# Performance work log

Measured on AMD Instinct MI355X. Metric: run time of the kernel, lower is better.

Reference implementation:

```python
import jax, jax.numpy as jnp
import numpy as np

B, T, N, CIN, C, L, NC, S = 8, 64, 200, 200, 128, 2, 2, 100
SPARSITY = 30


def bn(x, g, b, eps=1e-5):
    # BatchNorm1d forward with batch statistics (training-mode math, biased var)
    m = x.mean(0)
    v = x.var(0)
    return (x - m) / jnp.sqrt(v + eps) * g + b


def ln(x, g, b, eps=1e-5):
    m = x.mean(-1, keepdims=True)
    v = x.var(-1, keepdims=True)
    return (x - m) / jnp.sqrt(v + eps) * g + b


def setup_inputs() -> dict:
    key = jax.random.key(0)
    ks = iter(jax.random.split(key, 64))

    def nrm(shape, s=0.02):
        return jax.random.normal(next(ks), shape, jnp.float32) * s

    return dict(
        fMRI_v=jax.random.normal(next(ks), (B, T, N, CIN), jnp.float32),
        fMRI_a=jax.random.uniform(next(ks), (B, T, N, N), jnp.float32),
        sMRI_trad=jax.random.normal(next(ks), (B, S), jnp.float32),
        sMRI_deep=jnp.zeros((B, 1, 8, 8, 8), jnp.float32),
        csatt=1, CA_MOD=0,
        w_init=nrm((CIN, C)), b_init=jnp.zeros((C,), jnp.float32),
        gin_eps=jnp.zeros((L,), jnp.float32),
        gin_w1=nrm((L, C, C)), gin_b1=jnp.zeros((L, C), jnp.float32),
        gin_bn1_g=jnp.ones((L, C), jnp.float32), gin_bn1_b=jnp.zeros((L, C), jnp.float32),
        gin_w2=nrm((L, C, C)), gin_b2=jnp.zeros((L, C), jnp.float32),
        gin_bn2_g=jnp.ones((L, C), jnp.float32), gin_bn2_b=jnp.zeros((L, C), jnp.float32),
        sero_w=nrm((L, C, C)), sero_b=jnp.zeros((L, C), jnp.float32),
        sero_bn_g=jnp.ones((L, C), jnp.float32), sero_bn_b=jnp.zeros((L, C), jnp.float32),
        sero_aw=nrm((L, C, N)), sero_ab=jnp.zeros((L, N), jnp.float32),
        tr_wqkv=nrm((L, C, 3 * C)), tr_bqkv=jnp.zeros((L, 3 * C), jnp.float32),
        tr_wo=nrm((L, C, C)), tr_bo=jnp.zeros((L, C), jnp.float32),
        tr_ln1_g=jnp.ones((L, C), jnp.float32), tr_ln1_b=jnp.zeros((L, C), jnp.float32),
        tr_ln2_g=jnp.ones((L, C), jnp.float32), tr_ln2_b=jnp.zeros((L, C), jnp.float32),
        tr_w1=nrm((L, C, 2 * C)), tr_b1=jnp.zeros((L, 2 * C), jnp.float32),
        tr_w2=nrm((L, 2 * C, C)), tr_b2=jnp.zeros((L, C), jnp.float32),
        cls_w=nrm((L, C, NC)), cls_b=jnp.zeros((L, NC), jnp.float32),
        smri_w=nrm((S, C)), smri_b=jnp.zeros((C,), jnp.float32),
        smri_bn_g=jnp.ones((C,), jnp.float32), smri_bn_b=jnp.zeros((C,), jnp.float32),
    )


def reference(fMRI_v, fMRI_a, sMRI_trad, sMRI_deep, csatt, CA_MOD,
              w_init, b_init, gin_eps,
              gin_w1, gin_b1, gin_bn1_g, gin_bn1_b,
              gin_w2, gin_b2, gin_bn2_g, gin_bn2_b,
              sero_w, sero_b, sero_bn_g, sero_bn_b, sero_aw, sero_ab,
              tr_wqkv, tr_bqkv, tr_wo, tr_bo,
              tr_ln1_g, tr_ln1_b, tr_ln2_g, tr_ln2_b,
              tr_w1, tr_b1, tr_w2, tr_b2,
              cls_w, cls_b, smri_w, smri_b, smri_bn_g, smri_bn_b):
    b, t, n = fMRI_a.shape[:3]
    # initial linear over flattened (b t n) tokens
    h3 = (fMRI_v.reshape(-1, fMRI_v.shape[-1]) @ w_init + b_init).reshape(b, t, n, -1)
    # _collate_adjacency: per-(sample,timepoint) percentile threshold -> block-diag sparse
    # with all-ones values; equivalent to a batched masked matmul.
    thr = jnp.percentile(fMRI_a, 100 - SPARSITY, axis=(-2, -1), keepdims=True)
    mask = (fMRI_a > thr).astype(h3.dtype)  # [b,t,n,n]

    logit = jnp.zeros((b, cls_w.shape[-1]), h3.dtype)
    latents, node_attns, time_attns = [], [], []
    scale = 1.0 / jnp.sqrt(jnp.asarray(h3.shape[-1], h3.dtype))
    for l in range(L):
        # LayerGIN: note the original feeds h3 (initial features) to EVERY layer
        agg = jnp.einsum('btij,btjc->btic', mask, h3) + gin_eps[l] * h3
        x = agg.reshape(-1, agg.shape[-1])
        x = jax.nn.relu(bn(x @ gin_w1[l] + gin_b1[l], gin_bn1_g[l], gin_bn1_b[l]))
        x = jax.nn.relu(bn(x @ gin_w2[l] + gin_b2[l], gin_bn2_g[l], gin_bn2_b[l]))
        hb = x.reshape(b, t, n, -1).transpose(1, 0, 2, 3)  # (t,b,n,c)
        # ModuleSERO readout (node_axis=2)
        xr = hb.mean(2)  # (t,b,c)
        e = jax.nn.gelu(bn(xr.reshape(t * b, -1) @ sero_w[l] + sero_b[l],
                           sero_bn_g[l], sero_bn_b[l]), approximate=False)
        ga = jax.nn.sigmoid(e @ sero_aw[l] + sero_ab[l]).reshape(t, b, n)
        hr = (hb * ga[..., None]).mean(2)  # (t,b,c)
        node_attns.append(ga.transpose(1, 0, 2))  # (b,t,n)
        # ModuleTransformer (single head, post-LN, no residual before ln1)
        qkv = hr @ tr_wqkv[l] + tr_bqkv[l]
        q, k, v = jnp.split(qkv, 3, axis=-1)
        A = jax.nn.softmax(jnp.einsum('tbc,sbc->bts', q, k) * scale, axis=-1)  # (b,t,t)
        att = jnp.einsum('bts,sbc->tbc', A, v) @ tr_wo[l] + tr_bo[l]
        x1 = ln(att, tr_ln1_g[l], tr_ln1_b[l])
        m = jax.nn.relu(x1 @ tr_w1[l] + tr_b1[l]) @ tr_w2[l] + tr_b2[l]
        x2 = ln(x1 + m, tr_ln2_g[l], tr_ln2_b[l])
        time_attns.append(A)
        lat = x2.sum(0)  # cls_token='sum' over time
        logit = logit + lat @ cls_w[l] + cls_b[l]
        latents.append(lat)
    feat_fMRI = jnp.stack(latents, 1).mean(1)  # (b,c)
    feat_sMRI = bn(sMRI_trad @ smri_w + smri_b, smri_bn_g, smri_bn_b)
    node_attn = jnp.stack(node_attns, 1)  # (b,L,t,n)
    time_attn = jnp.stack(time_attns, 1)  # (b,L,t,t)
    return (logit, feat_fMRI, feat_sMRI, node_attn, time_attn)
```

## Files before the change

kernel.cpp:

```cpp
#include <hip/hip_runtime.h>
#include <math.h>

#define B_   8
#define T_   64
#define N_   200
#define CIN_ 200
#define C_   128
#define L_   2
#define NC_  2
#define S_   100
#define BT_  512
#define RB_  102400

typedef __attribute__((ext_vector_type(8))) short short8v;
typedef __attribute__((ext_vector_type(4))) float f32x4v;

union U4S8 { uint4 u; short8v s; };

__device__ __forceinline__ unsigned short f2bf(float f) {
    unsigned u = __float_as_uint(f);
    unsigned r = (u + 0x7FFFu + ((u >> 16) & 1u)) >> 16;
    return (unsigned short)r;
}
__device__ __forceinline__ float bf2f(unsigned short u) {
    return __uint_as_float(((unsigned)u) << 16);
}
__device__ __forceinline__ float bflo(unsigned u) { return __uint_as_float(u << 16); }
__device__ __forceinline__ float bfhi(unsigned u) { return __uint_as_float(u & 0xFFFF0000u); }
__device__ __forceinline__ unsigned packbf(float a, float b) {
    return (unsigned)f2bf(a) | ((unsigned)f2bf(b) << 16);
}

#define GLL(src, dst) __builtin_amdgcn_global_load_lds( \
    (const __attribute__((address_space(1))) unsigned int*)(src), \
    (__attribute__((address_space(3))) unsigned int*)(dst), 16, 0, 0)

__global__ __launch_bounds__(1024) void thr_kernel(const float* __restrict__ a,
                                                   float* __restrict__ thr,
                                                   unsigned* __restrict__ msk) {
    __shared__ int      hist[1024];
    __shared__ int      red[1024];
    __shared__ unsigned smask[1400];
    __shared__ float    candV[6144];
    __shared__ unsigned short candP[6144];
    __shared__ int      part[256];
    __shared__ int      grp[32];
    __shared__ float    cand2[256];
    __shared__ int      meta[8];
    __shared__ float    s_thr;
    int tid = threadIdx.x, lane = tid & 63;
    int bt = blockIdx.x;
    hist[tid] = 0;
    for (int i = tid; i < 1400; i += 1024) smask[i] = 0u;
    if (tid == 0) { meta[0] = 0; meta[1] = 0; }
    __syncthreads();

    const float4* x4 = (const float4*)(a + (long)bt * 40000);
    int c_lo = 0;
    #pragma unroll 1
    for (int it = 0; it < 10; it++) {
        int i4 = tid + it * 1024;
        unsigned nhi = 0u, ncm = 0u;
        float vv[4] = {0.f, 0.f, 0.f, 0.f};
        if (i4 < 10000) {
            float4 v = x4[i4];
            vv[0] = v.x; vv[1] = v.y; vv[2] = v.z; vv[3] = v.w;
            #pragma unroll
            for (int j = 0; j < 4; j++) {
                float f = vv[j];
                if (f < 0.65f) c_lo++;
                else if (f < 0.75f) ncm |= 1u << j;
                else nhi |= 1u << j;
            }
            if (nhi) {
                int vi = i4 * 4;
                int row = vi / 200, col = vi - row * 200;
                atomicOr(&smask[row * 7 + (col >> 5)], nhi << (col & 31));
            }
        }
        int cnt = __popc(ncm);
        int pfx = cnt;
        #pragma unroll
        for (int d = 1; d < 64; d <<= 1) {
            int t = __shfl_up(pfx, d, 64);
            if (lane >= d) pfx += t;
        }
        int total = __shfl(pfx, 63, 64);
        if (total) {
            int bw = 0;
            if (lane == 63) bw = atomicAdd(&meta[0], total);
            bw = __shfl(bw, 63, 64);
            int p = bw + pfx - cnt;
            #pragma unroll
            for (int j = 0; j < 4; j++) {
                if ((ncm >> j) & 1u) {
                    float f = vv[j];
                    if (p < 6144) { candV[p] = f; candP[p] = (unsigned short)(i4 * 4 + j); }
                    int bin = (int)((f - 0.65f) * 10240.0f);
                    bin = bin < 0 ? 0 : (bin > 1023 ? 1023 : bin);
                    atomicAdd(&hist[bin], 1);
                    p++;
                }
            }
        }
    }
    red[tid] = c_lo;
    __syncthreads();
    for (int off = 512; off; off >>= 1) {
        if (tid < off) red[tid] += red[tid + off];
        __syncthreads();
    }
    int c_lo_tot = red[0];
    if (tid < 256) part[tid] = hist[4*tid] + hist[4*tid+1] + hist[4*tid+2] + hist[4*tid+3];
    __syncthreads();
    if (tid < 32) {
        int s = 0;
        for (int i = 0; i < 8; i++) s += part[8*tid + i];
        grp[tid] = s;
    }
    __syncthreads();
    if (tid == 0) {
        int r = 27999 - c_lo_tot;
        int cum = 0, g = 0;
        while (cum + grp[g] <= r) cum += grp[g++];
        int t = g * 8;
        while (cum + part[t] <= r) cum += part[t++];
        int b = t * 4;
        while (cum + hist[b] <= r) cum += hist[b++];
        meta[2] = b; meta[3] = cum;
        int r1 = r + 1;
        cum = 0; g = 0;
        while (cum + grp[g] <= r1) cum += grp[g++];
        t = g * 8;
        while (cum + part[t] <= r1) cum += part[t++];
        b = t * 4;
        while (cum + hist[b] <= r1) cum += hist[b++];
        meta[4] = b; meta[5] = r;
    }
    __syncthreads();
    int blo = meta[2], base = meta[3], bhi = meta[4], r = meta[5];
    int m = meta[0]; if (m > 6144) m = 6144;
    for (int i = tid; i < m; i += 1024) {
        float v = candV[i];
        int bin = (int)((v - 0.65f) * 10240.0f);
        bin = bin < 0 ? 0 : (bin > 1023 ? 1023 : bin);
        if (bin >= blo && bin <= bhi) {
            int p = atomicAdd(&meta[1], 1);
            if (p < 256) cand2[p] = v;
        }
    }
    __syncthreads();
    if (tid == 0) {
        int m2 = meta[1]; if (m2 > 256) m2 = 256;
        for (int i = 1; i < m2; i++) {
            float key = cand2[i]; int j = i - 1;
            while (j >= 0 && cand2[j] > key) { cand2[j+1] = cand2[j]; j--; }
            cand2[j+1] = key;
        }
        float s1 = cand2[r - base], s2 = cand2[r + 1 - base];
        float tv = s1 * 0.701171875f + s2 * 0.298828125f;
        thr[bt] = tv;
        s_thr = tv;
    }
    __syncthreads();
    float tv = s_thr;
    for (int i = tid; i < m; i += 1024) {
        if (candV[i] > tv) {
            int vi = candP[i];
            int row = vi / 200, col = vi - row * 200;
            atomicOr(&smask[row * 7 + (col >> 5)], 1u << (col & 31));
        }
    }
    __syncthreads();
    for (int i = tid; i < 1400; i += 1024)
        msk[(long)bt * 1400 + i] = smask[i];
}

__global__ void wtcvt5_kernel(const float* __restrict__ w_init,
                              const float* __restrict__ gin_w1,
                              const float* __restrict__ gin_w2,
                              unsigned short* __restrict__ WT0,
                              unsigned short* __restrict__ WT1,
                              unsigned short* __restrict__ WT2) {
    int grp = blockIdx.x >> 7, c = blockIdx.x & 127;
    const float* w; unsigned short* wt; int K, Kpad;
    if (grp == 0)      { w = w_init;                     wt = WT0;                     K = 200; Kpad = 224; }
    else if (grp <= 2) { w = gin_w1 + (grp - 1) * C_ * C_; wt = WT1 + (grp - 1) * 128 * 128; K = 128; Kpad = 128; }
    else               { w = gin_w2 + (grp - 3) * C_ * C_; wt = WT2 + (grp - 3) * 128 * 128; K = 128; Kpad = 128; }
    for (int k = threadIdx.x; k < Kpad; k += 64)
        wt[(long)c * Kpad + k] = f2bf((k < K) ? w[(long)k * 128 + c] : 0.f);
}

__global__ __launch_bounds__(256) void bngemm_kernel(
        const unsigned short* __restrict__ xb,
        const unsigned short* __restrict__ wt,
        const float* __restrict__ bias, const float* __restrict__ statsIn,
        const float* __restrict__ bng, const float* __restrict__ bnb,
        unsigned short* __restrict__ y, float* __restrict__ statsOut) {
    __shared__ unsigned char pool[65536];
    __shared__ float bnS[128], bnB[128];
    int tid = threadIdx.x;
    int wave = tid >> 6, lane = tid & 63, quad = lane >> 4, m16 = lane & 15;
    long row0g = (long)blockIdx.x * 128;

    {
        int r0 = tid >> 2;
        int csw = (tid & 3) ^ ((r0 >> 1) & 3);
        int r1 = 64 + (tid >> 2);
        int csw1 = (tid & 3) ^ ((r1 >> 1) & 3);
        #pragma unroll
        for (int ks = 0; ks < 4; ks++) {
            char* Adst = (char*)pool + ks * 16384;
            char* Bdst = Adst + 8192;
            GLL((const char*)xb + ((row0g + r0) * 128 + ks * 32) * 2 + csw * 16,
                Adst + wave * 1024);
            GLL((const char*)xb + ((row0g + r1) * 128 + ks * 32) * 2 + csw1 * 16,
                Adst + 4096 + wave * 1024);
            GLL((const char*)wt + (long)r0 * 256 + ks * 64 + csw * 16,
                Bdst + wave * 1024);
            GLL((const char*)wt + (long)r1 * 256 + ks * 64 + csw1 * 16,
                Bdst + 4096 + wave * 1024);
        }
    }
    if (tid < 128) {
        float mm = statsIn[tid] * (1.f / (float)RB_);
        float var = fmaxf(statsIn[128 + tid] * (1.f / (float)RB_) - mm * mm, 0.f);
        float sc = bng[tid] / sqrtf(var + 1e-5f);
        bnS[tid] = sc; bnB[tid] = bnb[tid] - mm * sc;
    }
    f32x4v acc[2][8];
    #pragma unroll
    for (int i = 0; i < 2; i++)
        #pragma unroll
        for (int j = 0; j < 8; j++) acc[i][j] = (f32x4v){0.f, 0.f, 0.f, 0.f};

    __syncthreads();

    #pragma unroll 1
    for (int ks = 0; ks < 4; ks++) {
        const char* Ab = (const char*)pool + ks * 16384;
        const char* Bb = Ab + 8192;
        int kf = ks * 32 + quad * 8;
        U4S8 bU[8];
        #pragma unroll
        for (int nt = 0; nt < 8; nt++) {
            int r = nt * 16 + m16;
            int ch = quad ^ ((r >> 1) & 3);
            bU[nt].u = *(const uint4*)(Bb + r * 64 + ch * 16);
        }
        U4S8 aU[2];
        #pragma unroll
        for (int mt = 0; mt < 2; mt++) {
            int r = wave * 32 + mt * 16 + m16;
            int ch = quad ^ ((r >> 1) & 3);
            aU[mt].u = *(const uint4*)(Ab + r * 64 + ch * 16);
        }
        float4 s0 = *(const float4*)&bnS[kf], s1 = *(const float4*)&bnS[kf + 4];
        float4 b0 = *(const float4*)&bnB[kf], b1 = *(const float4*)&bnB[kf + 4];
        #pragma unroll
        for (int mt = 0; mt < 2; mt++) {
            uint4 u = aU[mt].u;
            float f0 = fmaxf(bflo(u.x) * s0.x + b0.x, 0.f);
            float f1 = fmaxf(bfhi(u.x) * s0.y + b0.y, 0.f);
            float f2 = fmaxf(bflo(u.y) * s0.z + b0.z, 0.f);
            float f3 = fmaxf(bfhi(u.y) * s0.w + b0.w, 0.f);
            float f4 = fmaxf(bflo(u.z) * s1.x + b1.x, 0.f);
            float f5 = fmaxf(bfhi(u.z) * s1.y + b1.y, 0.f);
            float f6 = fmaxf(bflo(u.w) * s1.z + b1.z, 0.f);
            float f7 = fmaxf(bfhi(u.w) * s1.w + b1.w, 0.f);
            u.x = packbf(f0, f1); u.y = packbf(f2, f3);
            u.z = packbf(f4, f5); u.w = packbf(f6, f7);
            aU[mt].u = u;
        }
        #pragma unroll
        for (int nt = 0; nt < 8; nt++) {
            acc[0][nt] = __builtin_amdgcn_mfma_f32_16x16x32_bf16(aU[0].s, bU[nt].s, acc[0][nt], 0, 0, 0);
            acc[1][nt] = __builtin_amdgcn_mfma_f32_16x16x32_bf16(aU[1].s, bU[nt].s, acc[1][nt], 0, 0, 0);
        }
    }

    __syncthreads();
    unsigned short* trans = (unsigned short*)pool;
    float sAcc[8], qAcc[8];
    #pragma unroll
    for (int nt = 0; nt < 8; nt++) {
        int col = nt * 16 + m16;
        float bv = bias[col];
        float s = 0.f, q = 0.f;
        #pragma unroll
        for (int mt = 0; mt < 2; mt++) {
            int lrb = wave * 32 + mt * 16 + quad * 4;
            #pragma unroll
            for (int i = 0; i < 4; i++) {
                int lr = lrb + i;
                float v = acc[mt][nt][i] + bv;
                trans[lr * 128 + (col ^ ((lr & 6) << 2))] = f2bf(v);
                s += v; q += v * v;
            }
        }
        sAcc[nt] = s; qAcc[nt] = q;
    }
    __syncthreads();
    #pragma unroll
    for (int rnd = 0; rnd < 8; rnd++) {
        int row = rnd * 16 + (tid >> 4), ch = tid & 15;
        uint4 v = *(const uint4*)&trans[row * 128 + ((ch * 8) ^ ((row & 6) << 2))];
        *(uint4*)&y[(row0g + row) * 128 + ch * 8] = v;
    }
    __syncthreads();
    float* redS = (float*)pool;
    float* redQ = redS + 2048;
    #pragma unroll
    for (int nt = 0; nt < 8; nt++) {
        int col = nt * 16 + m16;
        redS[col * 16 + wave * 4 + quad] = sAcc[nt];
        redQ[col * 16 + wave * 4 + quad] = qAcc[nt];
    }
    __syncthreads();
    if (tid < 128) {
        float s = 0.f, q = 0.f;
        #pragma unroll
        for (int j = 0; j < 16; j++) { s += redS[tid * 16 + j]; q += redQ[tid * 16 + j]; }
        atomicAdd(&statsOut[tid], s);
        atomicAdd(&statsOut[128 + tid], q);
    }
}

__global__ __launch_bounds__(256) void h3gemmT_kernel(
        const float* __restrict__ xv, const unsigned short* __restrict__ wt,
        const float* __restrict__ bias,
        unsigned short* __restrict__ yrow, unsigned short* __restrict__ zt) {
    __shared__ unsigned char pool[49152];
    int tid = threadIdx.x;
    int wave = tid >> 6, lane = tid & 63, quad = lane >> 4, m16 = lane & 15;
    long row0g = (long)blockIdx.x * 128;

    auto STAGE = [&](int buf, int ks) {
        #pragma unroll
        for (int j = 0; j < 2; j++) {
            int r = j * 64 + (tid >> 2);
            int c = (tid & 3) ^ ((r >> 1) & 3);
            const char* src = (const char*)wt + (long)r * 448 + ks * 64 + c * 16;
            char* dst = (char*)pool + 32768 + buf * 8192 + j * 4096 + wave * 1024;
            GLL(src, dst);
        }
        const char* xb = (const char*)xv;
        #pragma unroll
        for (int j = 0; j < 4; j++) {
            int r = j * 32 + (tid >> 3);
            int c = (tid & 7) ^ (r & 7);
            const char* src = xb + ((row0g + r) * 200 + ks * 32) * 4 + c * 16;
            char* dst = (char*)pool + buf * 16384 + j * 4096 + wave * 1024;
            GLL(src, dst);
        }
    };

    f32x4v acc[2][8];
    #pragma unroll
    for (int i = 0; i < 2; i++)
        #pragma unroll
        for (int j = 0; j < 8; j++) acc[i][j] = (f32x4v){0.f, 0.f, 0.f, 0.f};

    STAGE(0, 0);
    __syncthreads();

    for (int ks = 0; ks < 6; ks++) {
        if (ks + 1 < 6) {
            STAGE((ks + 1) & 1, ks + 1);
            asm volatile("s_waitcnt vmcnt(6)" ::: "memory");
        } else {
            asm volatile("s_waitcnt vmcnt(0)" ::: "memory");
        }
        __builtin_amdgcn_s_barrier();
        asm volatile("" ::: "memory");

        const char* Ab = (const char*)pool + (ks & 1) * 16384;
        const char* Bb = (const char*)pool + 32768 + (ks & 1) * 8192;
        U4S8 bU[8];
        #pragma unroll
        for (int nt = 0; nt < 8; nt++) {
            int r = nt * 16 + m16;
            int ch = quad ^ ((r >> 1) & 3);
            bU[nt].u = *(const uint4*)(Bb + r * 64 + ch * 16);
        }
        U4S8 aU[2];
        #pragma unroll
        for (int mt = 0; mt < 2; mt++) {
            int r = wave * 32 + mt * 16 + m16;
            int swz = r & 7;
            const char* base = Ab + r * 128;
            float4 v0 = *(const float4*)(base + ((2 * quad) ^ swz) * 16);
            float4 v1 = *(const float4*)(base + ((2 * quad + 1) ^ swz) * 16);
            uint4 o;
            o.x = packbf(v0.x, v0.y); o.y = packbf(v0.z, v0.w);
            o.z = packbf(v1.x, v1.y); o.w = packbf(v1.z, v1.w);
            aU[mt].u = o;
        }
        #pragma unroll
        for (int nt = 0; nt < 8; nt++) {
            acc[0][nt] = __builtin_amdgcn_mfma_f32_16x16x32_bf16(aU[0].s, bU[nt].s, acc[0][nt], 0, 0, 0);
            acc[1][nt] = __builtin_amdgcn_mfma_f32_16x16x32_bf16(aU[1].s, bU[nt].s, acc[1][nt], 0, 0, 0);
        }
        asm volatile("s_waitcnt lgkmcnt(0)" ::: "memory");
        __builtin_amdgcn_s_barrier();
        asm volatile("" ::: "memory");
    }
    {
        int kf = 192 + quad * 8;
        U4S8 bU[8];
        #pragma unroll
        for (int nt = 0; nt < 8; nt++)
            bU[nt].u = *(const uint4*)&wt[(long)(nt * 16 + m16) * 224 + kf];
        U4S8 aU[2];
        #pragma unroll
        for (int mt = 0; mt < 2; mt++) {
            uint4 o = {0u, 0u, 0u, 0u};
            if (kf + 8 <= 200) {
                const float* p = &xv[(row0g + wave * 32 + mt * 16 + m16) * 200 + kf];
                float4 v0 = *(const float4*)p;
                float4 v1 = *(const float4*)(p + 4);
                o.x = packbf(v0.x, v0.y); o.y = packbf(v0.z, v0.w);
                o.z = packbf(v1.x, v1.y); o.w = packbf(v1.z, v1.w);
            }
            aU[mt].u = o;
        }
        #pragma unroll
        for (int nt = 0; nt < 8; nt++) {
            acc[0][nt] = __builtin_amdgcn_mfma_f32_16x16x32_bf16(aU[0].s, bU[nt].s, acc[0][nt], 0, 0, 0);
            acc[1][nt] = __builtin_amdgcn_mfma_f32_16x16x32_bf16(aU[1].s, bU[nt].s, acc[1][nt], 0, 0, 0);
        }
    }

    unsigned short* tile = (unsigned short*)pool;
    #pragma unroll
    for (int nt = 0; nt < 8; nt++) {
        int col = nt * 16 + m16;
        float bv = bias[col];
        #pragma unroll
        for (int mt = 0; mt < 2; mt++) {
            int lrb = wave * 32 + mt * 16 + quad * 4;
            #pragma unroll
            for (int i = 0; i < 4; i++) {
                int lr = lrb + i;
                tile[lr * 128 + (col ^ ((lr & 14) << 2))] = f2bf(acc[mt][nt][i] + bv);
            }
        }
    }
    __syncthreads();
    #pragma unroll
    for (int rnd = 0; rnd < 8; rnd++) {
        int row = rnd * 16 + (tid >> 4), ch = tid & 15;
        uint4 v = *(const uint4*)&tile[row * 128 + ((ch * 8) ^ ((row & 14) << 2))];
        *(uint4*)&yrow[(row0g + row) * 128 + ch * 8] = v;
    }
    int r0 = blockIdx.x * 128;
    int bt0 = r0 / 200, n0 = r0 - bt0 * 200;
    int len0 = 200 - n0; if (len0 > 128) len0 = 128;
    int c = tid & 127, h = tid >> 7;
    #pragma unroll
    for (int u = 0; u < 8; u++) {
        int rl = h * 64 + u * 8;
        unsigned short e[8];
        #pragma unroll
        for (int j = 0; j < 8; j++)
            e[j] = tile[(rl + j) * 128 + (c ^ (((rl + j) & 14) << 2))];
        uint4 o;
        o.x = (unsigned)e[0] | ((unsigned)e[1] << 16);
        o.y = (unsigned)e[2] | ((unsigned)e[3] << 16);
        o.z = (unsigned)e[4] | ((unsigned)e[5] << 16);
        o.w = (unsigned)e[6] | ((unsigned)e[7] << 16);
        int bt, n;
        if (rl < len0) { bt = bt0; n = n0 + rl; } else { bt = bt0 + 1; n = rl - len0; }
        *(uint4*)&zt[((long)bt * 128 + c) * 224 + n] = o;
    }
    if (n0 >= 72) {
        uint4 z = {0u, 0u, 0u, 0u};
        for (int idx = tid; idx < 384; idx += 256) {
            int c2 = idx & 127, u2 = idx >> 7;
            *(uint4*)&zt[((long)bt0 * 128 + c2) * 224 + 200 + u2 * 8] = z;
        }
    }
}

__global__ __launch_bounds__(256) void maskfused_kernel(
        const unsigned* __restrict__ msk, const unsigned short* __restrict__ zt,
        const unsigned short* __restrict__ h3, const unsigned short* __restrict__ w1t,
        const float* __restrict__ geps, int l, const float* __restrict__ b1,
        unsigned short* __restrict__ y, float* __restrict__ statsOut) {
    __shared__ unsigned char pool[65536];
    __shared__ unsigned sbits[128 * 7];
    int tid = threadIdx.x;
    int bt = blockIdx.x & 511, half = blockIdx.x >> 9;
    int row0 = half * 128;
    int wave = tid >> 6, lane = tid & 63, quad = lane >> 4, m16 = lane & 15;
    const char* ztb = (const char*)(zt + (long)bt * 128 * 224);

    {
        int r0 = tid >> 2;
        int q0 = (tid & 3) ^ ((r0 >> 1) & 3);
        int r1 = 64 + (tid >> 2);
        int q1 = (tid & 3) ^ ((r1 >> 1) & 3);
        #pragma unroll
        for (int kc = 0; kc < 7; kc++) {
            char* dst = (char*)pool + kc * 8192;
            GLL(ztb + r0 * 448 + kc * 64 + q0 * 16, dst + wave * 1024);
            GLL(ztb + r1 * 448 + kc * 64 + q1 * 16, dst + 4096 + wave * 1024);
        }
    }
    for (int idx = tid; idx < 896; idx += 256) {
        int gr = row0 + idx / 7;
        sbits[idx] = (gr < N_) ? msk[(long)bt * 1400 + gr * 7 + (idx % 7)] : 0u;
    }
    unsigned ONEu = 0x3F80u;

    f32x4v acc[2][8];
    #pragma unroll
    for (int i = 0; i < 2; i++)
        #pragma unroll
        for (int j = 0; j < 8; j++) acc[i][j] = (f32x4v){0.f, 0.f, 0.f, 0.f};

    __syncthreads();

    #pragma unroll 1
    for (int kc = 0; kc < 7; kc++) {
        const char* sb = (const char*)pool + kc * 8192;
        U4S8 bU[8];
        #pragma unroll
        for (int nt = 0; nt < 8; nt++) {
            int r = nt * 16 + m16;
            int q = quad ^ ((r >> 1) & 3);
            bU[nt].u = *(const uint4*)(sb + r * 64 + q * 16);
        }
        U4S8 aU[2];
        #pragma unroll
        for (int mt = 0; mt < 2; mt++) {
            int lr = wave * 32 + mt * 16 + m16;
            unsigned bits = (sbits[lr * 7 + kc] >> (quad * 8)) & 0xFFu;
            unsigned o[4];
            #pragma unroll
            for (int p = 0; p < 4; p++) {
                unsigned lo = ((bits >> (2 * p)) & 1u) ? ONEu : 0u;
                unsigned hi = ((bits >> (2 * p + 1)) & 1u) ? ONEu : 0u;
                o[p] = lo | (hi << 16);
            }
            aU[mt].u = make_uint4(o[0], o[1], o[2], o[3]);
        }
        #pragma unroll
        for (int nt = 0; nt < 8; nt++) {
            acc[0][nt] = __builtin_amdgcn_mfma_f32_16x16x32_bf16(aU[0].s, bU[nt].s, acc[0][nt], 0, 0, 0);
            acc[1][nt] = __builtin_amdgcn_mfma_f32_16x16x32_bf16(aU[1].s, bU[nt].s, acc[1][nt], 0, 0, 0);
        }
    }
    __syncthreads();

    unsigned short* magg = (unsigned short*)pool;
    unsigned short* trans = (unsigned short*)(pool + 32768);
    #pragma unroll
    for (int nt = 0; nt < 8; nt++) {
        int col = nt * 16 + m16;
        #pragma unroll
        for (int mt = 0; mt < 2; mt++) {
            int lrb = wave * 32 + mt * 16 + quad * 4;
            #pragma unroll
            for (int i = 0; i < 4; i++) {
                int lr = lrb + i;
                magg[lr * 128 + (col ^ ((lr & 6) << 2))] = f2bf(acc[mt][nt][i]);
            }
        }
    }
    __syncthreads();

    float eps = geps[l];
    f32x4v acc2[2][8];
    #pragma unroll
    for (int i = 0; i < 2; i++)
        #pragma unroll
        for (int j = 0; j < 8; j++) acc2[i][j] = (f32x4v){0.f, 0.f, 0.f, 0.f};

    #pragma unroll 1
    for (int ks = 0; ks < 4; ks++) {
        int kf = ks * 32 + quad * 8;
        U4S8 bU[8];
        #pragma unroll
        for (int nt = 0; nt < 8; nt++)
            bU[nt].u = *(const uint4*)&w1t[(long)(nt * 16 + m16) * 128 + kf];
        U4S8 aU[2];
        #pragma unroll
        for (int mt = 0; mt < 2; mt++) {
            int r = wave * 32 + mt * 16 + m16;
            uint4 mu = *(const uint4*)&magg[r * 128 + (kf ^ ((r & 6) << 2))];
            int gr = row0 + r;
            uint4 hu = {0u, 0u, 0u, 0u};
            if (gr < N_) hu = *(const uint4*)&h3[((long)bt * N_ + gr) * 128 + kf];
            float f0 = bflo(mu.x) + eps * bflo(hu.x);
            float f1 = bfhi(mu.x) + eps * bfhi(hu.x);
            float f2 = bflo(mu.y) + eps * bflo(hu.y);
            float f3 = bfhi(mu.y) + eps * bfhi(hu.y);
            float f4 = bflo(mu.z) + eps * bflo(hu.z);
            float f5 = bfhi(mu.z) + eps * bfhi(hu.z);
            float f6 = bflo(mu.w) + eps * bflo(hu.w);
            float f7 = bfhi(mu.w) + eps * bfhi(hu.w);
            uint4 o;
            o.x = packbf(f0, f1); o.y = packbf(f2, f3);
            o.z = packbf(f4, f5); o.w = packbf(f6, f7);
            aU[mt].u = o;
        }
        #pragma unroll
        for (int nt = 0; nt < 8; nt++) {
            acc2[0][nt] = __builtin_amdgcn_mfma_f32_16x16x32_bf16(aU[0].s, bU[nt].s, acc2[0][nt], 0, 0, 0);
            acc2[1][nt] = __builtin_amdgcn_mfma_f32_16x16x32_bf16(aU[1].s, bU[nt].s, acc2[1][nt], 0, 0, 0);
        }
    }

    float sAcc[8], qAcc[8];
    #pragma unroll
    for (int nt = 0; nt < 8; nt++) {
        int col = nt * 16 + m16;
        float bv = b1[col];
        float s = 0.f, q = 0.f;
        #pragma unroll
        for (int mt = 0; mt < 2; mt++) {
            int lrb = wave * 32 + mt * 16 + quad * 4;
            #pragma unroll
            for (int i = 0; i < 4; i++) {
                int lr = lrb + i;
                float v = acc2[mt][nt][i] + bv;
                trans[lr * 128 + (col ^ ((lr & 6) << 2))] = f2bf(v);
                if (row0 + lr < N_) { s += v; q += v * v; }
            }
        }
        sAcc[nt] = s; qAcc[nt] = q;
    }
    __syncthreads();
    #pragma unroll
    for (int rnd = 0; rnd < 8; rnd++) {
        int row = rnd * 16 + (tid >> 4), ch = tid & 15;
        int gr = row0 + row;
        uint4 v = *(const uint4*)&trans[row * 128 + ((ch * 8) ^ ((row & 6) << 2))];
        if (gr < N_)
            *(uint4*)&y[((long)bt * N_ + gr) * 128 + ch * 8] = v;
    }
    __syncthreads();
    float* redS = (float*)(pool + 32768);
    float* redQ = redS + 2048;
    #pragma unroll
    for (int nt = 0; nt < 8; nt++) {
        int col = nt * 16 + m16;
        redS[col * 16 + wave * 4 + quad] = sAcc[nt];
        redQ[col * 16 + wave * 4 + quad] = qAcc[nt];
    }
    __syncthreads();
    if (tid < 128) {
        float s = 0.f, q = 0.f;
        #pragma unroll
        for (int j = 0; j < 16; j++) { s += redS[tid * 16 + j]; q += redQ[tid * 16 + j]; }
        atomicAdd(&statsOut[tid], s);
        atomicAdd(&statsOut[128 + tid], q);
    }
}

__global__ __launch_bounds__(256) void xrE_kernel(
        const unsigned short* __restrict__ raw, const float* __restrict__ stats,
        const float* __restrict__ g, const float* __restrict__ b,
        const float* __restrict__ sw, const float* __restrict__ sb,
        float* __restrict__ E, float* __restrict__ statE) {
    __shared__ float red[256];
    __shared__ float xrrow[128];
    int tid = threadIdx.x, c = tid & 127, hf = tid >> 7;
    int t = blockIdx.x / B_, bb = blockIdx.x % B_;
    const unsigned short* base = raw + ((long)bb * T_ + t) * N_ * C_;
    float m = stats[c] * (1.f / (float)RB_);
    float var = fmaxf(stats[128 + c] * (1.f / (float)RB_) - m * m, 0.f);
    float sc = g[c] / sqrtf(var + 1e-5f);
    float sh = b[c] - m * sc;
    float s = 0.f;
    for (int n = hf * 100; n < hf * 100 + 100; n++)
        s += fmaxf(fmaf(bf2f(base[n * C_ + c]), sc, sh), 0.f);
    red[tid] = s;
    __syncthreads();
    if (hf == 0) xrrow[c] = (red[c] + red[c + 128]) * (1.f / 200.f);
    __syncthreads();
    float acc = 0.f;
    for (int k = hf * 64; k < hf * 64 + 64; k++)
        acc = fmaf(xrrow[k], sw[k * C_ + c], acc);
    red[tid] = acc;
    __syncthreads();
    if (hf == 0) {
        float v = red[c] + red[c + 128] + sb[c];
        E[(long)blockIdx.x * C_ + c] = v;
        atomicAdd(&statE[c], v);
        atomicAdd(&statE[C_ + c], v * v);
    }
}

__global__ __launch_bounds__(256) void ga_kernel(const float* __restrict__ eRaw,
                          const float* __restrict__ stats,
                          const float* __restrict__ sg, const float* __restrict__ sb,
                          const float* __restrict__ aw, const float* __restrict__ ab,
                          float* __restrict__ ga, float* __restrict__ node_out, int l) {
    __shared__ float sx[4 * C_];
    __shared__ float bnS[C_], bnB[C_];
    int tid = threadIdx.x;
    if (tid < C_) {
        float m = stats[tid] * (1.f / (float)BT_);
        float var = fmaxf(stats[C_ + tid] * (1.f / (float)BT_) - m * m, 0.f);
        float inv = 1.f / sqrtf(var + 1e-5f);
        float sc = inv * sg[tid];
        bnS[tid] = sc;
        bnB[tid] = sb[tid] - m * sc;
    }
    __syncthreads();
    long r0 = (long)blockIdx.x * 4;
    for (int idx = tid; idx < 4 * C_; idx += 256) {
        int col = idx & (C_ - 1);
        float v = eRaw[r0 * C_ + idx] * bnS[col] + bnB[col];
        sx[idx] = 0.5f * v * (1.f + erff(v * 0.70710678118654752f));
    }
    __syncthreads();
    int c = tid;
    if (c < N_) {
        float acc[4] = {0.f, 0.f, 0.f, 0.f};
        for (int k = 0; k < C_; k++) {
            float wv = aw[k * N_ + c];
            #pragma unroll
            for (int i = 0; i < 4; i++) acc[i] = fmaf(sx[i * C_ + k], wv, acc[i]);
        }
        float bv = ab[c];
        for (int i = 0; i < 4; i++) {
            int tb = (int)r0 + i;
            int t = tb / B_, b = tb % B_;
            float v = 1.f / (1.f + expf(-(acc[i] + bv)));
            ga[(long)tb * N_ + c] = v;
            node_out[(((long)b * L_ + l) * T_ + t) * N_ + c] = v;
        }
    }
}

__global__ __launch_bounds__(256) void hrQKV_kernel(
        const unsigned short* __restrict__ raw, const float* __restrict__ stats,
        const float* __restrict__ g, const float* __restrict__ b,
        const float* __restrict__ ga, const float* __restrict__ wq,
        const float* __restrict__ bq, float* __restrict__ qkv) {
    __shared__ float sga[N_];
    __shared__ float red[256];
    __shared__ float hrrow[128];
    int tid = threadIdx.x, c = tid & 127, hf = tid >> 7;
    int t = blockIdx.x / B_, bb = blockIdx.x % B_;
    const unsigned short* base = raw + ((long)bb * T_ + t) * N_ * C_;
    for (int i = tid; i < N_; i += 256) sga[i] = ga[(long)blockIdx.x * N_ + i];
    __syncthreads();
    float m = stats[c] * (1.f / (float)RB_);
    float var = fmaxf(stats[128 + c] * (1.f / (float)RB_) - m * m, 0.f);
    float sc = g[c] / sqrtf(var + 1e-5f);
    float sh = b[c] - m * sc;
    float s = 0.f;
    for (int n = hf * 100; n < hf * 100 + 100; n++)
        s = fmaf(fmaxf(fmaf(bf2f(base[n * C_ + c]), sc, sh), 0.f), sga[n], s);
    red[tid] = s;
    __syncthreads();
    if (hf == 0) hrrow[c] = (red[c] + red[c + 128]) * (1.f / 200.f);
    __syncthreads();
    for (int out = tid; out < 384; out += 256) {
        float acc = 0.f;
        for (int k = 0; k < C_; k++)
            acc = fmaf(hrrow[k], wq[k * 384 + out], acc);
        qkv[(long)blockIdx.x * 384 + out] = acc + bq[out];
    }
}

__global__ __launch_bounds__(128) void attnln_kernel(const float* __restrict__ qkv,
        const float* __restrict__ wo, const float* __restrict__ bo,
        const float* __restrict__ g, const float* __restrict__ bb,
        float* __restrict__ time_out, float* __restrict__ x1, int l) {
    __shared__ float q[C_];
    __shared__ float sa[T_];
    __shared__ float av[C_];
    __shared__ float red[C_];
    int tid = threadIdx.x;
    int t = blockIdx.x / B_, b = blockIdx.x % B_;
    q[tid] = qkv[((long)t * B_ + b) * 384 + tid];
    __syncthreads();
    if (tid < 64) {
        const float* krow = qkv + ((long)tid * B_ + b) * 384 + C_;
        float s = 0.f;
        for (int c = 0; c < C_; c++) s = fmaf(q[c], krow[c], s);
        s *= 0.08838834764831843f;
        float mx = s;
        #pragma unroll
        for (int off = 32; off; off >>= 1) mx = fmaxf(mx, __shfl_xor(mx, off));
        float e = expf(s - mx), sum = e;
        #pragma unroll
        for (int off = 32; off; off >>= 1) sum += __shfl_xor(sum, off);
        float p = e / sum;
        sa[tid] = p;
        time_out[(((long)b * L_ + l) * T_ + t) * T_ + tid] = p;
    }
    __syncthreads();
    float s2 = 0.f;
    for (int sp = 0; sp < T_; sp++)
        s2 = fmaf(sa[sp], qkv[((long)sp * B_ + b) * 384 + 256 + tid], s2);
    av[tid] = s2;
    __syncthreads();
    float a0 = 0.f;
    for (int k = 0; k < C_; k++) a0 = fmaf(av[k], wo[k * C_ + tid], a0);
    float v = a0 + bo[tid];
    red[tid] = v; __syncthreads();
    for (int off = 64; off; off >>= 1) { if (tid < off) red[tid] += red[tid + off]; __syncthreads(); }
    float m = red[0] * (1.f / C_); __syncthreads();
    float d = v - m;
    red[tid] = d * d; __syncthreads();
    for (int off = 64; off; off >>= 1) { if (tid < off) red[tid] += red[tid + off]; __syncthreads(); }
    float var = red[0] * (1.f / C_);
    x1[(long)blockIdx.x * C_ + tid] = d * (1.f / sqrtf(var + 1e-5f)) * g[tid] + bb[tid];
}

__global__ __launch_bounds__(256) void ffn_kernel(const float* __restrict__ x1,
                          const float* __restrict__ w1, const float* __restrict__ b1,
                          const float* __restrict__ w2, const float* __restrict__ b2,
                          const float* __restrict__ g, const float* __restrict__ bb,
                          float* __restrict__ lat) {
    __shared__ float sx[2 * C_];
    __shared__ float mid[2 * 256];
    __shared__ float red[C_];
    int tid = threadIdx.x;
    long r0 = (long)blockIdx.x * 2;
    sx[tid] = x1[r0 * C_ + tid];
    __syncthreads();
    float a0 = 0.f, a1 = 0.f;
    for (int k = 0; k < C_; k++) {
        float wv = w1[k * 256 + tid];
        a0 = fmaf(sx[k], wv, a0);
        a1 = fmaf(sx[C_ + k], wv, a1);
    }
    float bv = b1[tid];
    mid[tid]       = fmaxf(a0 + bv, 0.f);
    mid[256 + tid] = fmaxf(a1 + bv, 0.f);
    __syncthreads();
    float v[2] = {0.f, 0.f};
    if (tid < C_) {
        float c0 = 0.f, c1 = 0.f;
        for (int k = 0; k < 256; k++) {
            float wv = w2[k * C_ + tid];
            c0 = fmaf(mid[k], wv, c0);
            c1 = fmaf(mid[256 + k], wv, c1);
        }
        float bv2 = b2[tid];
        v[0] = c0 + bv2 + sx[tid];
        v[1] = c1 + bv2 + sx[C_ + tid];
    }
    #pragma unroll 1
    for (int r = 0; r < 2; r++) {
        if (tid < C_) red[tid] = v[r];
        __syncthreads();
        for (int off = 64; off; off >>= 1) { if (tid < off) red[tid] += red[tid + off]; __syncthreads(); }
        float m = red[0] * (1.f / C_); __syncthreads();
        float d = v[r] - m;
        if (tid < C_) red[tid] = d * d;
        __syncthreads();
        for (int off = 64; off; off >>= 1) { if (tid < off) red[tid] += red[tid + off]; __syncthreads(); }
        float var = red[0] * (1.f / C_); __syncthreads();
        if (tid < C_) {
            float outv = d * (1.f / sqrtf(var + 1e-5f)) * g[tid] + bb[tid];
            int b = (int)((r0 + r) % B_);
            atomicAdd(&lat[b * C_ + tid], outv);
        }
    }
}

__global__ void final_kernel(const float* __restrict__ lat, const float* __restrict__ cls_w,
                             const float* __restrict__ cls_b, float* __restrict__ out) {
    int idx = blockIdx.x * blockDim.x + threadIdx.x;
    if (idx < B_ * NC_) {
        int b = idx / NC_, nc = idx % NC_;
        float s = 0.f;
        for (int l = 0; l < L_; l++) {
            float acc = 0.f;
            for (int c = 0; c < C_; c++)
                acc = fmaf(lat[l * B_ * C_ + b * C_ + c], cls_w[l * C_ * NC_ + c * NC_ + nc], acc);
            s += acc + cls_b[l * NC_ + nc];
        }
        out[idx] = s;
    } else if (idx < B_ * NC_ + B_ * C_) {
        int j = idx - B_ * NC_;
        out[idx] = 0.5f * (lat[j] + lat[B_ * C_ + j]);
    }
}

__global__ void smri_kernel(const float* __restrict__ trad, const float* __restrict__ w,
                            const float* __restrict__ bias, const float* __restrict__ g,
                            const float* __restrict__ bb, float* __restrict__ out) {
    int c = threadIdx.x;
    float y[B_];
    for (int b = 0; b < B_; b++) {
        float s = bias[c];
        for (int k = 0; k < S_; k++) s = fmaf(trad[b * S_ + k], w[k * C_ + c], s);
        y[b] = s;
    }
    float m = 0.f;
    for (int b = 0; b < B_; b++) m += y[b];
    m *= (1.f / B_);
    float var = 0.f;
    for (int b = 0; b < B_; b++) { float d = y[b] - m; var += d * d; }
    var *= (1.f / B_);
    float inv = 1.f / sqrtf(var + 1e-5f);
    for (int b = 0; b < B_; b++) out[b * C_ + c] = (y[b] - m) * inv * g[c] + bb[c];
}

extern "C" void kernel_launch(void* const* d_in, const int* in_sizes, int n_in,
                              void* d_out, int out_size, void* d_ws, size_t ws_size,
                              hipStream_t stream) {
    const float* fv       = (const float*)d_in[0];
    const float* fa       = (const float*)d_in[1];
    const float* trad     = (const float*)d_in[2];
    const float* w_init   = (const float*)d_in[6];
    const float* b_init   = (const float*)d_in[7];
    const float* gin_eps  = (const float*)d_in[8];
    const float* gin_w1   = (const float*)d_in[9];
    const float* gin_b1   = (const float*)d_in[10];
    const float* gbn1g    = (const float*)d_in[11];
    const float* gbn1b    = (const float*)d_in[12];
    const float* gin_w2   = (const float*)d_in[13];
    const float* gin_b2   = (const float*)d_in[14];
    const float* gbn2g    = (const float*)d_in[15];
    const float* gbn2b    = (const float*)d_in[16];
    const float* sero_w   = (const float*)d_in[17];
    const float* sero_b   = (const float*)d_in[18];
    const float* sbng     = (const float*)d_in[19];
    const float* sbnb     = (const float*)d_in[20];
    const float* sero_aw  = (const float*)d_in[21];
    const float* sero_ab  = (const float*)d_in[22];
    const float* wqkv     = (const float*)d_in[23];
    const float* bqkv     = (const float*)d_in[24];
    const float* wo       = (const float*)d_in[25];
    const float* bo       = (const float*)d_in[26];
    const float* ln1g     = (const float*)d_in[27];
    const float* ln1b     = (const float*)d_in[28];
    const float* ln2g     = (const float*)d_in[29];
    const float* ln2b     = (const float*)d_in[30];
    const float* tw1      = (const float*)d_in[31];
    const float* tb1      = (const float*)d_in[32];
    const float* tw2      = (const float*)d_in[33];
    const float* tb2      = (const float*)d_in[34];
    const float* cls_w    = (const float*)d_in[35];
    const float* cls_b    = (const float*)d_in[36];
    const float* smri_w   = (const float*)d_in[37];
    const float* smri_b   = (const float*)d_in[38];
    const float* smri_g   = (const float*)d_in[39];
    const float* smri_bb  = (const float*)d_in[40];

    float* out = (float*)d_out;

    const long SZ_BIG = (long)RB_ * C_;
    unsigned short* H3b = (unsigned short*)d_ws;
    unsigned short* Y1b = H3b + SZ_BIG;
    unsigned short* Y2b = Y1b + SZ_BIG;
    unsigned short* ZTb = Y2b + SZ_BIG;
    float* fbase = (float*)(ZTb + (long)BT_ * 128 * 224);
    float* THR  = fbase;
    float* SBUF = THR + 512;
    float* LAT  = SBUF + 1536;
    float* E    = LAT + 2048;
    float* GA   = E + BT_ * C_;
    float* QKV  = GA + BT_ * N_;
    float* X1   = QKV + BT_ * 3 * C_;
    unsigned short* WT0 = (unsigned short*)(X1 + BT_ * C_);
    unsigned short* WT1 = WT0 + 128 * 224;
    unsigned short* WT2 = WT1 + 2 * 128 * 128;
    unsigned* MSK = (unsigned*)(WT2 + 2 * 128 * 128);

    float* OUT_LOGIT = out;
    float* OUT_FEATS = out + 1040;
    float* OUT_NODE  = out + 2064;
    float* OUT_TIME  = out + 206864;

    wtcvt5_kernel<<<640, 64, 0, stream>>>(w_init, gin_w1, gin_w2, WT0, WT1, WT2);
    hipMemsetAsync(SBUF, 0, (1536 + 2048) * sizeof(float), stream);

    h3gemmT_kernel<<<RB_ / 128, 256, 0, stream>>>(fv, WT0, b_init, H3b, ZTb);
    thr_kernel<<<BT_, 1024, 0, stream>>>(fa, THR, MSK);

    for (int l = 0; l < L_; l++) {
        float* SA = SBUF + l * 768;
        float* SB = SA + 256;
        float* SE = SA + 512;
        maskfused_kernel<<<BT_ * 2, 256, 0, stream>>>(MSK, ZTb, H3b, WT1 + l * 128 * 128,
            gin_eps, l, gin_b1 + l * C_, Y2b, SA);
        bngemm_kernel<<<RB_ / 128, 256, 0, stream>>>(
            Y2b, WT2 + l * 128 * 128, gin_b2 + l * C_, SA,
            gbn1g + l * C_, gbn1b + l * C_, Y1b, SB);
        xrE_kernel<<<BT_, 256, 0, stream>>>(Y1b, SB, gbn2g + l * C_, gbn2b + l * C_,
            sero_w + l * C_ * C_, sero_b + l * C_, E, SE);
        ga_kernel<<<BT_ / 4, 256, 0, stream>>>(E, SE, sbng + l * C_, sbnb + l * C_,
            sero_aw + l * C_ * N_, sero_ab + l * N_, GA, OUT_NODE, l);
        hrQKV_kernel<<<BT_, 256, 0, stream>>>(Y1b, SB, gbn2g + l * C_, gbn2b + l * C_,
            GA, wqkv + l * C_ * 3 * C_, bqkv + l * 3 * C_, QKV);
        attnln_kernel<<<BT_, 128, 0, stream>>>(QKV, wo + l * C_ * C_, bo + l * C_,
            ln1g + l * C_, ln1b + l * C_, OUT_TIME, X1, l);
        ffn_kernel<<<BT_ / 2, 256, 0, stream>>>(X1, tw1 + l * C_ * 2 * C_, tb1 + l * 2 * C_,
            tw2 + l * 2 * C_ * C_, tb2 + l * C_, ln2g + l * C_, ln2b + l * C_,
            LAT + l * B_ * C_);
    }

    final_kernel<<<5, 256, 0, stream>>>(LAT, cls_w, cls_b, OUT_LOGIT);
    smri_kernel<<<1, 128, 0, stream>>>(trad, smri_w, smri_b, smri_g, smri_bb, OUT_FEATS);
}
```

Baseline: 706.0 us.

## Batch per-layer readout and transformer kernels across both layers into single launches

The two GIN layers still run in sequence, but each of the small downstream kernels (SERO readout, gating, QKV, attention/LN, FFN) now launches once for both layers. The block index selects the layer, which doubles the grid of each launch and removes five launches. Per-layer intermediates get separate buffers, carved from workspace regions (ZTb, MSK) that are dead by the time they are written. This trades extra workspace aliasing, which could go wrong if sizes or lifetimes are off, for better GPU fill and less launch overhead on the latency-bound small kernels.

```diff
diff --git a/kernel.cpp b/kernel.cpp
--- a/kernel.cpp
+++ b/kernel.cpp
@@ -659,15 +659,25 @@
     }
 }
 
-__global__ __launch_bounds__(256) void xrE_kernel(
-        const unsigned short* __restrict__ raw, const float* __restrict__ stats,
-        const float* __restrict__ g, const float* __restrict__ b,
-        const float* __restrict__ sw, const float* __restrict__ sb,
-        float* __restrict__ E, float* __restrict__ statE) {
+__global__ __launch_bounds__(256) void xrE2_kernel(
+        const unsigned short* __restrict__ raw0, const unsigned short* __restrict__ raw1,
+        const float* __restrict__ SBUF,
+        const float* __restrict__ gall, const float* __restrict__ ball,
+        const float* __restrict__ swall, const float* __restrict__ sball,
+        float* __restrict__ E0, float* __restrict__ E1, float* __restrict__ statBase) {
     __shared__ float red[256];
     __shared__ float xrrow[128];
+    int l = blockIdx.x >> 9, tb = blockIdx.x & 511;
+    const unsigned short* raw = l ? raw1 : raw0;
+    const float* stats = SBUF + l * 768 + 256;
+    const float* g = gall + l * C_;
+    const float* b = ball + l * C_;
+    const float* sw = swall + l * C_ * C_;
+    const float* sb = sball + l * C_;
+    float* E = l ? E1 : E0;
+    float* statE = (float*)statBase + l * 768 + 512;
     int tid = threadIdx.x, c = tid & 127, hf = tid >> 7;
-    int t = blockIdx.x / B_, bb = blockIdx.x % B_;
+    int t = tb / B_, bb = tb % B_;
     const unsigned short* base = raw + ((long)bb * T_ + t) * N_ * C_;
     float m = stats[c] * (1.f / (float)RB_);
     float var = fmaxf(stats[128 + c] * (1.f / (float)RB_) - m * m, 0.f);
@@ -687,19 +697,29 @@
     __syncthreads();
     if (hf == 0) {
         float v = red[c] + red[c + 128] + sb[c];
-        E[(long)blockIdx.x * C_ + c] = v;
+        E[(long)tb * C_ + c] = v;
         atomicAdd(&statE[c], v);
         atomicAdd(&statE[C_ + c], v * v);
     }
 }
 
-__global__ __launch_bounds__(256) void ga_kernel(const float* __restrict__ eRaw,
-                          const float* __restrict__ stats,
-                          const float* __restrict__ sg, const float* __restrict__ sb,
-                          const float* __restrict__ aw, const float* __restrict__ ab,
-                          float* __restrict__ ga, float* __restrict__ node_out, int l) {
+__global__ __launch_bounds__(256) void ga2_kernel(
+        const float* __restrict__ E0f, const float* __restrict__ E1f,
+        const float* __restrict__ SBUF,
+        const float* __restrict__ sgall, const float* __restrict__ sball,
+        const float* __restrict__ awall, const float* __restrict__ aball,
+        float* __restrict__ GA0, float* __restrict__ GA1,
+        float* __restrict__ node_out) {
     __shared__ float sx[4 * C_];
     __shared__ float bnS[C_], bnB[C_];
+    int l = blockIdx.x >> 7, sub = blockIdx.x & 127;
+    const float* eRaw = l ? E1f : E0f;
+    const float* stats = SBUF + l * 768 + 512;
+    const float* sg = sgall + l * C_;
+    const float* sb = sball + l * C_;
+    const float* aw = awall + l * C_ * N_;
+    const float* ab = aball + l * N_;
+    float* ga = l ? GA1 : GA0;
     int tid = threadIdx.x;
     if (tid < C_) {
         float m = stats[tid] * (1.f / (float)BT_);
@@ -710,7 +730,7 @@
         bnB[tid] = sb[tid] - m * sc;
     }
     __syncthreads();
-    long r0 = (long)blockIdx.x * 4;
+    long r0 = (long)sub * 4;
     for (int idx = tid; idx < 4 * C_; idx += 256) {
         int col = idx & (C_ - 1);
         float v = eRaw[r0 * C_ + idx] * bnS[col] + bnB[col];
@@ -736,18 +756,29 @@
     }
 }
 
-__global__ __launch_bounds__(256) void hrQKV_kernel(
-        const unsigned short* __restrict__ raw, const float* __restrict__ stats,
-        const float* __restrict__ g, const float* __restrict__ b,
-        const float* __restrict__ ga, const float* __restrict__ wq,
-        const float* __restrict__ bq, float* __restrict__ qkv) {
+__global__ __launch_bounds__(256) void hrQKV2_kernel(
+        const unsigned short* __restrict__ raw0, const unsigned short* __restrict__ raw1,
+        const float* __restrict__ SBUF,
+        const float* __restrict__ gall, const float* __restrict__ ball,
+        const float* __restrict__ GA0, const float* __restrict__ GA1,
+        const float* __restrict__ wqall, const float* __restrict__ bqall,
+        float* __restrict__ QKV0, float* __restrict__ QKV1) {
     __shared__ float sga[N_];
     __shared__ float red[256];
     __shared__ float hrrow[128];
+    int l = blockIdx.x >> 9, tb = blockIdx.x & 511;
+    const unsigned short* raw = l ? raw1 : raw0;
+    const float* stats = SBUF + l * 768 + 256;
+    const float* g = gall + l * C_;
+    const float* b = ball + l * C_;
+    const float* ga = l ? GA1 : GA0;
+    const float* wq = wqall + (long)l * C_ * 3 * C_;
+    const float* bq = bqall + l * 3 * C_;
+    float* qkv = l ? QKV1 : QKV0;
     int tid = threadIdx.x, c = tid & 127, hf = tid >> 7;
-    int t = blockIdx.x / B_, bb = blockIdx.x % B_;
+    int t = tb / B_, bb = tb % B_;
     const unsigned short* base = raw + ((long)bb * T_ + t) * N_ * C_;
-    for (int i = tid; i < N_; i += 256) sga[i] = ga[(long)blockIdx.x * N_ + i];
+    for (int i = tid; i < N_; i += 256) sga[i] = ga[(long)tb * N_ + i];
     __syncthreads();
     float m = stats[c] * (1.f / (float)RB_);
     float var = fmaxf(stats[128 + c] * (1.f / (float)RB_) - m * m, 0.f);
@@ -764,20 +795,28 @@
         float acc = 0.f;
         for (int k = 0; k < C_; k++)
             acc = fmaf(hrrow[k], wq[k * 384 + out], acc);
-        qkv[(long)blockIdx.x * 384 + out] = acc + bq[out];
-    }
-}
-
-__global__ __launch_bounds__(128) void attnln_kernel(const float* __restrict__ qkv,
-        const float* __restrict__ wo, const float* __restrict__ bo,
-        const float* __restrict__ g, const float* __restrict__ bb,
-        float* __restrict__ time_out, float* __restrict__ x1, int l) {
+        qkv[(long)tb * 384 + out] = acc + bq[out];
+    }
+}
+
+__global__ __launch_bounds__(128) void attnln2_kernel(
+        const float* __restrict__ QKV0, const float* __restrict__ QKV1,
+        const float* __restrict__ woall, const float* __restrict__ boall,
+        const float* __restrict__ gall, const float* __restrict__ ball,
+        float* __restrict__ time_out, float* __restrict__ X10, float* __restrict__ X11) {
     __shared__ float q[C_];
     __shared__ float sa[T_];
     __shared__ float av[C_];
     __shared__ float red[C_];
+    int l = blockIdx.x >> 9, tb = blockIdx.x & 511;
+    const float* qkv = l ? QKV1 : QKV0;
+    const float* wo = woall + (long)l * C_ * C_;
+    const float* bo = boall + l * C_;
+    const float* g = gall + l * C_;
+    const float* bb = ball + l * C_;
+    float* x1 = l ? X11 : X10;
     int tid = threadIdx.x;
-    int t = blockIdx.x / B_, b = blockIdx.x % B_;
+    int t = tb / B_, b = tb % B_;
     q[tid] = qkv[((long)t * B_ + b) * 384 + tid];
     __syncthreads();
     if (tid < 64) {
@@ -811,19 +850,29 @@
     red[tid] = d * d; __syncthreads();
     for (int off = 64; off; off >>= 1) { if (tid < off) red[tid] += red[tid + off]; __syncthreads(); }
     float var = red[0] * (1.f / C_);
-    x1[(long)blockIdx.x * C_ + tid] = d * (1.f / sqrtf(var + 1e-5f)) * g[tid] + bb[tid];
-}
-
-__global__ __launch_bounds__(256) void ffn_kernel(const float* __restrict__ x1,
-                          const float* __restrict__ w1, const float* __restrict__ b1,
-                          const float* __restrict__ w2, const float* __restrict__ b2,
-                          const float* __restrict__ g, const float* __restrict__ bb,
-                          float* __restrict__ lat) {
+    x1[((long)t * B_ + b) * C_ + tid] = d * (1.f / sqrtf(var + 1e-5f)) * g[tid] + bb[tid];
+}
+
+__global__ __launch_bounds__(256) void ffn2_kernel(
+        const float* __restrict__ X10, const float* __restrict__ X11,
+        const float* __restrict__ w1all, const float* __restrict__ b1all,
+        const float* __restrict__ w2all, const float* __restrict__ b2all,
+        const float* __restrict__ gall, const float* __restrict__ ball,
+        float* __restrict__ LAT) {
     __shared__ float sx[2 * C_];
     __shared__ float mid[2 * 256];
     __shared__ float red[C_];
+    int l = blockIdx.x >> 8, sub = blockIdx.x & 255;
+    const float* x1 = l ? X11 : X10;
+    const float* w1 = w1all + (long)l * C_ * 2 * C_;
+    const float* b1 = b1all + l * 2 * C_;
+    const float* w2 = w2all + (long)l * 2 * C_ * C_;
+    const float* b2 = b2all + l * C_;
+    const float* g = gall + l * C_;
+    const float* bb = ball + l * C_;
+    float* lat = LAT + l * B_ * C_;
     int tid = threadIdx.x;
-    long r0 = (long)blockIdx.x * 2;
+    long r0 = (long)sub * 2;
     sx[tid] = x1[r0 * C_ + tid];
     __syncthreads();
     float a0 = 0.f, a1 = 0.f;
@@ -951,22 +1000,27 @@
     float* out = (float*)d_out;
 
     const long SZ_BIG = (long)RB_ * C_;
-    unsigned short* H3b = (unsigned short*)d_ws;
-    unsigned short* Y1b = H3b + SZ_BIG;
-    unsigned short* Y2b = Y1b + SZ_BIG;
-    unsigned short* ZTb = Y2b + SZ_BIG;
+    unsigned short* H3b  = (unsigned short*)d_ws;
+    unsigned short* Y1b0 = H3b + SZ_BIG;
+    unsigned short* Y2b  = Y1b0 + SZ_BIG;
+    unsigned short* ZTb  = Y2b + SZ_BIG;
+    unsigned short* Y1b1 = ZTb;
     float* fbase = (float*)(ZTb + (long)BT_ * 128 * 224);
     float* THR  = fbase;
     float* SBUF = THR + 512;
     float* LAT  = SBUF + 1536;
-    float* E    = LAT + 2048;
-    float* GA   = E + BT_ * C_;
-    float* QKV  = GA + BT_ * N_;
-    float* X1   = QKV + BT_ * 3 * C_;
-    unsigned short* WT0 = (unsigned short*)(X1 + BT_ * C_);
+    float* E0   = LAT + 2048;
+    float* GA0  = E0 + BT_ * C_;
+    float* QKV0 = GA0 + BT_ * N_;
+    float* X10  = QKV0 + BT_ * 3 * C_;
+    unsigned short* WT0 = (unsigned short*)(X10 + BT_ * C_);
     unsigned short* WT1 = WT0 + 128 * 224;
     unsigned short* WT2 = WT1 + 2 * 128 * 128;
     unsigned* MSK = (unsigned*)(WT2 + 2 * 128 * 128);
+    float* E1   = (float*)MSK;
+    float* GA1  = E1 + BT_ * C_;
+    float* QKV1 = GA1 + BT_ * N_;
+    float* X11  = QKV1 + BT_ * 3 * C_;
 
     float* OUT_LOGIT = out;
     float* OUT_FEATS = out + 1040;
@@ -979,27 +1033,26 @@
     h3gemmT_kernel<<<RB_ / 128, 256, 0, stream>>>(fv, WT0, b_init, H3b, ZTb);
     thr_kernel<<<BT_, 1024, 0, stream>>>(fa, THR, MSK);
 
-    for (int l = 0; l < L_; l++) {
-        float* SA = SBUF + l * 768;
-        float* SB = SA + 256;
-        float* SE = SA + 512;
-        maskfused_kernel<<<BT_ * 2, 256, 0, stream>>>(MSK, ZTb, H3b, WT1 + l * 128 * 128,
-            gin_eps, l, gin_b1 + l * C_, Y2b, SA);
-        bngemm_kernel<<<RB_ / 128, 256, 0, stream>>>(
-            Y2b, WT2 + l * 128 * 128, gin_b2 + l * C_, SA,
-            gbn1g + l * C_, gbn1b + l * C_, Y1b, SB);
-        xrE_kernel<<<BT_, 256, 0, stream>>>(Y1b, SB, gbn2g + l * C_, gbn2b + l * C_,
-            sero_w + l * C_ * C_, sero_b + l * C_, E, SE);
-        ga_kernel<<<BT_ / 4, 256, 0, stream>>>(E, SE, sbng + l * C_, sbnb + l * C_,
-            sero_aw + l * C_ * N_, sero_ab + l * N_, GA, OUT_NODE, l);
-        hrQKV_kernel<<<BT_, 256, 0, stream>>>(Y1b, SB, gbn2g + l * C_, gbn2b + l * C_,
-            GA, wqkv + l * C_ * 3 * C_, bqkv + l * 3 * C_, QKV);
-        attnln_kernel<<<BT_, 128, 0, stream>>>(QKV, wo + l * C_ * C_, bo + l * C_,
-            ln1g + l * C_, ln1b + l * C_, OUT_TIME, X1, l);
-        ffn_kernel<<<BT_ / 2, 256, 0, stream>>>(X1, tw1 + l * C_ * 2 * C_, tb1 + l * 2 * C_,
-            tw2 + l * 2 * C_ * C_, tb2 + l * C_, ln2g + l * C_, ln2b + l * C_,
-            LAT + l * B_ * C_);
-    }
+    maskfused_kernel<<<BT_ * 2, 256, 0, stream>>>(MSK, ZTb, H3b, WT1,
+        gin_eps, 0, gin_b1, Y2b, SBUF);
+    bngemm_kernel<<<RB_ / 128, 256, 0, stream>>>(
+        Y2b, WT2, gin_b2, SBUF, gbn1g, gbn1b, Y1b0, SBUF + 256);
+    maskfused_kernel<<<BT_ * 2, 256, 0, stream>>>(MSK, ZTb, H3b, WT1 + 128 * 128,
+        gin_eps, 1, gin_b1 + C_, Y2b, SBUF + 768);
+    bngemm_kernel<<<RB_ / 128, 256, 0, stream>>>(
+        Y2b, WT2 + 128 * 128, gin_b2 + C_, SBUF + 768, gbn1g + C_, gbn1b + C_,
+        Y1b1, SBUF + 768 + 256);
+
+    xrE2_kernel<<<2 * BT_, 256, 0, stream>>>(Y1b0, Y1b1, SBUF, gbn2g, gbn2b,
+        sero_w, sero_b, E0, E1, SBUF);
+    ga2_kernel<<<2 * (BT_ / 4), 256, 0, stream>>>(E0, E1, SBUF, sbng, sbnb,
+        sero_aw, sero_ab, GA0, GA1, OUT_NODE);
+    hrQKV2_kernel<<<2 * BT_, 256, 0, stream>>>(Y1b0, Y1b1, SBUF, gbn2g, gbn2b,
+        GA0, GA1, wqkv, bqkv, QKV0, QKV1);
+    attnln2_kernel<<<2 * BT_, 128, 0, stream>>>(QKV0, QKV1, wo, bo, ln1g, ln1b,
+        OUT_TIME, X10, X11);
+    ffn2_kernel<<<2 * (BT_ / 2), 256, 0, stream>>>(X10, X11, tw1, tb1, tw2, tb2,
+        ln2g, ln2b, LAT);
 
     final_kernel<<<5, 256, 0, stream>>>(LAT, cls_w, cls_b, OUT_LOGIT);
     smri_kernel<<<1, 128, 0, stream>>>(trad, smri_w, smri_b, smri_g, smri_bb, OUT_FEATS);
```

New measurement: 626.2 us. 11.3% less time.
